# Optimization experiments

Measured on AMD Instinct MI355X. Metric: run time of the kernel, lower is better.

## Reference

```python
import jax, jax.numpy as jnp
import numpy as np

H = 32          # num_attention_heads
KVH = 8         # num_key_value_heads
D = 2048        # hidden_size
HD = D // H     # attention_head_size = 64
REP = H // KVH  # queries per kv head = 4


def setup_inputs() -> dict:
    key = jax.random.key(0)
    ks = jax.random.split(key, 7)
    s = 0.02
    return {
        "hidden_states": jax.random.normal(ks[0], (2, 2048, D), dtype=jnp.float32),
        "Wq": jax.random.normal(ks[1], (D, D), dtype=jnp.float32) * s,
        "bq": jax.random.normal(ks[2], (D,), dtype=jnp.float32) * s,
        "Wk": jax.random.normal(ks[3], (D, KVH * HD), dtype=jnp.float32) * s,
        "bk": jax.random.normal(ks[4], (KVH * HD,), dtype=jnp.float32) * s,
        "Wv": jax.random.normal(ks[5], (D, KVH * HD), dtype=jnp.float32) * s,
        "bv": jax.random.normal(ks[6], (KVH * HD,), dtype=jnp.float32) * s,
    }


def _split_heads(x, n_heads):
    # [B, S, n_heads*HD] -> [B, n_heads, S, HD]
    b, s, _ = x.shape
    return x.reshape(b, s, n_heads, HD).transpose(0, 2, 1, 3)


def reference(hidden_states, Wq, bq, Wk, bk, Wv, bv):
    b, s, _ = hidden_states.shape
    q = _split_heads(hidden_states @ Wq + bq, H)          # [B,H,S,HD]
    k = _split_heads(hidden_states @ Wk + bk, KVH)        # [B,KVH,S,HD]
    v = _split_heads(hidden_states @ Wv + bv, KVH)
    # repeat KV heads to match query heads (q_idx // REP -> kv_idx)
    k = jnp.repeat(k, REP, axis=1)                         # [B,H,S,HD]
    v = jnp.repeat(v, REP, axis=1)
    scores = jnp.einsum("bhqd,bhkd->bhqk", q, k) / jnp.sqrt(jnp.float32(HD))
    probs = jax.nn.softmax(scores, axis=-1)
    ctx = jnp.einsum("bhqk,bhkd->bhqd", probs, v)          # [B,H,S,HD]
    ctx = ctx.transpose(0, 2, 1, 3).reshape(b, s, H * HD)
    return ctx
```

## Files before the change

### kernel.cpp

```cpp
#include <hip/hip_runtime.h>
#include <hip/hip_bf16.h>

#define NH 32
#define NKVH 8
#define DMODEL 2048
#define HDIM 64
#define NB 2
#define SEQ 2048
#define MROWS (NB*SEQ)
#define NQ 2048
#define NKV 512
#define NTOT 3072
#define NT (SEQ/64)

typedef __bf16 bf16x4 __attribute__((ext_vector_type(4)));
typedef __bf16 bf16x8 __attribute__((ext_vector_type(8)));
typedef float  f32x2  __attribute__((ext_vector_type(2)));
typedef float  f32x4  __attribute__((ext_vector_type(4)));
typedef float  f32x16 __attribute__((ext_vector_type(16)));
typedef unsigned u32x2 __attribute__((ext_vector_type(2)));
typedef unsigned u32x4 __attribute__((ext_vector_type(4)));

__device__ inline __bf16 f2bf(float f) {
    unsigned u = __builtin_bit_cast(unsigned, f);
    u += 0x7fff + ((u >> 16) & 1);
    unsigned short s = (unsigned short)(u >> 16);
    return __builtin_bit_cast(__bf16, s);
}

__device__ inline unsigned pack2bf(float a, float b) {
    unsigned ua = __builtin_bit_cast(unsigned, a);
    ua += 0x7fff + ((ua >> 16) & 1);
    unsigned ub = __builtin_bit_cast(unsigned, b);
    ub += 0x7fff + ((ub >> 16) & 1);
    return (ua >> 16) | (ub & 0xffff0000u);
}

__device__ inline void gload_lds16(const void* g, void* l) {
    __builtin_amdgcn_global_load_lds(
        (const __attribute__((address_space(1))) void*)g,
        (__attribute__((address_space(3))) void*)l, 16, 0, 0);
}

__device__ inline float max3f(float a, float b, float c) {
    float r;
    asm("v_max3_f32 %0, %1, %2, %3" : "=v"(r) : "v"(a), "v"(b), "v"(c));
    return r;
}

__device__ inline float cross_max32(float x) {
#if __has_builtin(__builtin_amdgcn_permlane32_swap)
    unsigned xu = __builtin_bit_cast(unsigned, x);
    u32x2 r = __builtin_amdgcn_permlane32_swap(xu, xu, false, false);
    return fmaxf(__builtin_bit_cast(float, r[0]), __builtin_bit_cast(float, r[1]));
#else
    return fmaxf(x, __shfl_xor(x, 32));
#endif
}

__global__ __launch_bounds__(256)
void cvt_hs(const float* __restrict__ Hs, __bf16* __restrict__ Ab)
{
    size_t idx = ((size_t)blockIdx.x * 256 + threadIdx.x) * 8;
    f32x4 a = *reinterpret_cast<const f32x4*>(Hs + idx);
    f32x4 b = *reinterpret_cast<const f32x4*>(Hs + idx + 4);
    u32x4 w;
    w[0] = pack2bf(a[0], a[1]); w[1] = pack2bf(a[2], a[3]);
    w[2] = pack2bf(b[0], b[1]); w[3] = pack2bf(b[2], b[3]);
    *reinterpret_cast<u32x4*>((char*)Ab + idx * 2) = w;
}

__global__ __launch_bounds__(256)
void transpose_w(const float* __restrict__ Wq,
                 const float* __restrict__ Wk,
                 const float* __restrict__ Wv,
                 __bf16* __restrict__ Wt)
{
    __shared__ __bf16 tile[64][72];
    int k0 = blockIdx.x * 64;
    int n0 = blockIdx.y * 64;
    const float* Wsrc; int ncols; int nbase;
    if (n0 < NQ)            { Wsrc = Wq; ncols = NQ;  nbase = n0; }
    else if (n0 < NQ + NKV) { Wsrc = Wk; ncols = NKV; nbase = n0 - NQ; }
    else                    { Wsrc = Wv; ncols = NKV; nbase = n0 - NQ - NKV; }
    int t = threadIdx.x;
    int kl = t >> 2;
    int nc = (t & 3) * 16;
    const float* src = Wsrc + (size_t)(k0 + kl) * ncols + nbase + nc;
    #pragma unroll
    for (int i = 0; i < 4; ++i) {
        f32x4 v = *reinterpret_cast<const f32x4*>(src + i * 4);
        #pragma unroll
        for (int e = 0; e < 4; ++e) tile[kl][nc + i * 4 + e] = f2bf(v[e]);
    }
    __syncthreads();
    int nl = t >> 2;
    int kc = (t & 3) * 16;
    bf16x8 o0, o1;
    #pragma unroll
    for (int i = 0; i < 8; ++i) o0[i] = tile[kc + i][nl];
    #pragma unroll
    for (int i = 0; i < 8; ++i) o1[i] = tile[kc + 8 + i][nl];
    __bf16* dst = Wt + (size_t)(n0 + nl) * DMODEL + k0 + kc;
    *reinterpret_cast<bf16x8*>(dst)     = o0;
    *reinterpret_cast<bf16x8*>(dst + 8) = o1;
}

#define BM 128
#define BN 128
#define BK 64

__global__ __launch_bounds__(256)
void qkv_gemm(const __bf16* __restrict__ Ab,
              const __bf16* __restrict__ Wt,
              const float* __restrict__ bq,
              const float* __restrict__ bk,
              const float* __restrict__ bv,
              __bf16* __restrict__ Qb,
              __bf16* __restrict__ Kb,
              __bf16* __restrict__ Vt)
{
    __shared__ char lds[32768];

    int bid = blockIdx.x;
    int wg = (bid & 7) * 96 + (bid >> 3);
    int n0 = (wg % 24) * BN;
    int m0 = (wg / 24) * BM;

    int t = threadIdx.x;
    int wave = t >> 6, lane = t & 63;
    int g = lane >> 4, lh = lane & 15;
    int wr = wave >> 1, wc = wave & 1;

    int srow = wave * 8 + (lane >> 3);
    int schunk = (lane & 7) ^ (lane >> 3);
    const char* Asrc = (const char*)Ab + (size_t)(m0 + srow) * 4096 + schunk * 16;
    const char* Bsrc = (const char*)Wt + (size_t)(n0 + srow) * 4096 + schunk * 16;
    int dstw = wave * 1024;

    f32x4 acc[4][4] = {};

    for (int k0 = 0; k0 < DMODEL * 2; k0 += BK * 2) {
        #pragma unroll
        for (int i = 0; i < 4; ++i)
            gload_lds16(Asrc + (size_t)i * 32 * 4096 + k0, lds + i * 4096 + dstw);
        #pragma unroll
        for (int i = 0; i < 4; ++i)
            gload_lds16(Bsrc + (size_t)i * 32 * 4096 + k0, lds + 16384 + i * 4096 + dstw);
        __syncthreads();
        #pragma unroll
        for (int kk = 0; kk < 2; ++kk) {
            bf16x8 af[4], bfr[4];
            #pragma unroll
            for (int mi = 0; mi < 4; ++mi) {
                int row = wr * 64 + mi * 16 + lh;
                int byte = row * 128 + (((kk * 4 + g) ^ (lh & 7)) << 4);
                af[mi] = *reinterpret_cast<const bf16x8*>(lds + byte);
            }
            #pragma unroll
            for (int ni = 0; ni < 4; ++ni) {
                int row = wc * 64 + ni * 16 + lh;
                int byte = row * 128 + (((kk * 4 + g) ^ (lh & 7)) << 4);
                bfr[ni] = *reinterpret_cast<const bf16x8*>(lds + 16384 + byte);
            }
            #pragma unroll
            for (int mi = 0; mi < 4; ++mi)
                #pragma unroll
                for (int ni = 0; ni < 4; ++ni)
                    acc[mi][ni] = __builtin_amdgcn_mfma_f32_16x16x32_bf16(af[mi], bfr[ni], acc[mi][ni], 0, 0, 0);
        }
        __syncthreads();
    }

    int mode = (n0 < NQ) ? 0 : (n0 < NQ + NKV ? 1 : 2);
    const float* bias = (mode == 0) ? bq : (mode == 1 ? bk : bv);
    int nsub = (mode == 0) ? 0 : (mode == 1 ? NQ : NQ + NKV);
    float scale = (mode == 0) ? 0.18033688011112042f : 1.0f;

    float biasv[4];
    #pragma unroll
    for (int ni = 0; ni < 4; ++ni)
        biasv[ni] = bias[n0 - nsub + wc * 64 + ni * 16 + lh];

    int gsw = ((g & 1) << 1) | (g >> 1);

    #pragma unroll
    for (int mi = 0; mi < 4; ++mi) {
        #pragma unroll
        for (int j = 0; j < 4; ++j) {
            int m = m0 + wr * 64 + mi * 16 + 4 * g + j;
            int bb = m >> 11, s = m & (SEQ - 1);
            #pragma unroll
            for (int ni = 0; ni < 4; ++ni) {
                int n = n0 + wc * 64 + ni * 16 + lh;
                __bf16 val = f2bf((acc[mi][ni][j] + biasv[ni]) * scale);
                if (mode == 0) {
                    int hh = n >> 6, d = n & 63;
                    Qb[(((size_t)bb * NH + hh) * SEQ + s) * HDIM + d] = val;
                } else if (mode == 1) {
                    int nk = n - NQ; int kv = nk >> 6, d = nk & 63;
                    Kb[(((size_t)bb * NKVH + kv) * SEQ + s) * HDIM + d] = val;
                } else {
                    int nv = n - NQ - NKV; int kv = nv >> 6, d = nv & 63;
                    int sv = (s & ~12) | (gsw << 2);
                    Vt[(((size_t)bb * NKVH + kv) * HDIM + d) * SEQ + sv] = val;
                }
            }
        }
    }
}

#define SUBSTEP(BUFB, SS) do { \
    bf16x8 kf0_ = *reinterpret_cast<const bf16x8*>(lds + (BUFB) + koff[(SS)*4 + 0]); \
    bf16x8 kf1_ = *reinterpret_cast<const bf16x8*>(lds + (BUFB) + koff[(SS)*4 + 1]); \
    bf16x8 kf2_ = *reinterpret_cast<const bf16x8*>(lds + (BUFB) + koff[(SS)*4 + 2]); \
    bf16x8 kf3_ = *reinterpret_cast<const bf16x8*>(lds + (BUFB) + koff[(SS)*4 + 3]); \
    f32x16 s_ = {}; \
    __builtin_amdgcn_s_setprio(1); \
    s_ = __builtin_amdgcn_mfma_f32_32x32x16_bf16(kf0_, qf[0], s_, 0, 0, 0); \
    s_ = __builtin_amdgcn_mfma_f32_32x32x16_bf16(kf1_, qf[1], s_, 0, 0, 0); \
    s_ = __builtin_amdgcn_mfma_f32_32x32x16_bf16(kf2_, qf[2], s_, 0, 0, 0); \
    s_ = __builtin_amdgcn_mfma_f32_32x32x16_bf16(kf3_, qf[3], s_, 0, 0, 0); \
    __builtin_amdgcn_s_setprio(0); \
    float n0_ = max3f(max3f(s_[0], s_[1], s_[2]),  max3f(s_[3], s_[4], s_[5]), \
                      max3f(s_[6], s_[7], s_[8])); \
    float n1_ = max3f(max3f(s_[9], s_[10], s_[11]), max3f(s_[12], s_[13], s_[14]), s_[15]); \
    float mt_ = cross_max32(fmaxf(n0_, n1_)); \
    if (!__all(mt_ <= m_run + 8.0f)) { \
        float mn_ = fmaxf(m_run, mt_); \
        float al_ = __builtin_amdgcn_exp2f(m_run - mn_); \
        m_run = mn_; msub = -mn_; \
        accO0 *= al_; accO1 *= al_; lsum *= al_; \
    } \
    _Pragma("unroll") \
    for (int r = 0; r < 16; ++r) s_[r] = __builtin_amdgcn_exp2f(s_[r] + msub); \
    bf16x8 pa_, pb_; \
    _Pragma("unroll") \
    for (int e = 0; e < 8; ++e) { pa_[e] = (__bf16)s_[e]; pb_[e] = (__bf16)s_[8 + e]; } \
    bf16x8 va0_ = *reinterpret_cast<const bf16x8*>(lds + (BUFB) + 8192 + koff[2 * (SS)]); \
    bf16x8 vb0_ = *reinterpret_cast<const bf16x8*>(lds + (BUFB) + 8192 + koff[2 * (SS) + 1]); \
    bf16x8 va1_ = *reinterpret_cast<const bf16x8*>(lds + (BUFB) + 8192 + koff[4 + 2 * (SS)]); \
    bf16x8 vb1_ = *reinterpret_cast<const bf16x8*>(lds + (BUFB) + 8192 + koff[4 + 2 * (SS) + 1]); \
    __builtin_amdgcn_s_setprio(1); \
    accO0 = __builtin_amdgcn_mfma_f32_32x32x16_bf16(va0_, pa_, accO0, 0, 0, 0); \
    lsum  = __builtin_amdgcn_mfma_f32_32x32x16_bf16(ones, pa_, lsum,  0, 0, 0); \
    accO0 = __builtin_amdgcn_mfma_f32_32x32x16_bf16(vb0_, pb_, accO0, 0, 0, 0); \
    lsum  = __builtin_amdgcn_mfma_f32_32x32x16_bf16(ones, pb_, lsum,  0, 0, 0); \
    accO1 = __builtin_amdgcn_mfma_f32_32x32x16_bf16(va1_, pa_, accO1, 0, 0, 0); \
    accO1 = __builtin_amdgcn_mfma_f32_32x32x16_bf16(vb1_, pb_, accO1, 0, 0, 0); \
    __builtin_amdgcn_s_setprio(0); \
} while (0)

#define TILE(BUFB, NBUFB, KT, MORE) do { \
    if (MORE) { \
        gload_lds16(Kp + (size_t)((KT) + 1) * 8192 + kgoff, lds + (NBUFB) + kdst); \
        gload_lds16(Vp + (size_t)((KT) + 1) * 128 + vgoff,  lds + (NBUFB) + vdst); \
    } \
    SUBSTEP(BUFB, 0); \
    SUBSTEP(BUFB, 1); \
    __syncthreads(); \
} while (0)

__global__ __launch_bounds__(512, 4)
void attn(const __bf16* __restrict__ Qb,
          const __bf16* __restrict__ Kb,
          const __bf16* __restrict__ Vt,
          float* __restrict__ out)
{
    __shared__ char lds[32768];

    int qt = blockIdx.x;
    int bh = blockIdx.y;
    int b = bh >> 5, h = bh & 31;
    int kvh = h >> 2;
    int tid = threadIdx.x, wave = tid >> 6, lane = tid & 63;
    int ql = lane & 31, hi = lane >> 5;
    int q0 = qt * 256 + wave * 32;

    const __bf16* Qp = Qb + (size_t)(b * NH + h) * SEQ * HDIM;
    const char*   Kp = (const char*)(Kb + (size_t)(b * NKVH + kvh) * SEQ * HDIM);
    const char*   Vp = (const char*)(Vt + (size_t)(b * NKVH + kvh) * HDIM * SEQ);

    bf16x8 qf[4];
    #pragma unroll
    for (int f = 0; f < 4; ++f)
        qf[f] = *reinterpret_cast<const bf16x8*>(Qp + (size_t)(q0 + ql) * HDIM + f * 16 + hi * 8);

    u32x4 ou = { 0x3F803F80u, 0x3F803F80u, 0x3F803F80u, 0x3F803F80u };
    bf16x8 ones = __builtin_bit_cast(bf16x8, ou);

    int srow = tid >> 3;
    int schk = (tid & 7) ^ (srow & 7);
    int kgoff = srow * 128 + (schk << 4);
    size_t vgoff = (size_t)srow * (SEQ * 2) + (schk << 4);
    int kdst = tid * 16;
    int vdst = 8192 + tid * 16;

    int koff[8];
    #pragma unroll
    for (int kb = 0; kb < 2; ++kb)
        #pragma unroll
        for (int f = 0; f < 4; ++f)
            koff[kb * 4 + f] = (kb * 32 + ql) * 128 + ((f * 32 + hi * 16) ^ ((ql & 7) << 4));

    f32x16 accO0 = {}, accO1 = {}, lsum = {};
    float m_run = -1e30f, msub = 0.0f;

    gload_lds16(Kp + kgoff, lds + kdst);
    gload_lds16(Vp + vgoff, lds + vdst);
    __syncthreads();

    #pragma unroll 1
    for (int kt2 = 0; kt2 < 15; ++kt2) {
        TILE(0,     16384, 2 * kt2,     true);
        TILE(16384, 0,     2 * kt2 + 1, true);
    }
    TILE(0,     16384, 30, true);
    TILE(16384, 0,     31, false);

    float inv = 1.0f / lsum[0];
    float* op = out + ((size_t)b * SEQ + q0 + ql) * DMODEL + h * HDIM;
    #pragma unroll
    for (int G = 0; G < 4; ++G) {
        f32x4 o0 = { accO0[4 * G + 0] * inv, accO0[4 * G + 1] * inv,
                     accO0[4 * G + 2] * inv, accO0[4 * G + 3] * inv };
        f32x4 o1 = { accO1[4 * G + 0] * inv, accO1[4 * G + 1] * inv,
                     accO1[4 * G + 2] * inv, accO1[4 * G + 3] * inv };
        *reinterpret_cast<f32x4*>(op + 8 * G + 4 * hi)      = o0;
        *reinterpret_cast<f32x4*>(op + 32 + 8 * G + 4 * hi) = o1;
    }
}

extern "C" void kernel_launch(void* const* d_in, const int* in_sizes, int n_in,
                              void* d_out, int out_size, void* d_ws, size_t ws_size,
                              hipStream_t stream)
{
    const float* hs = (const float*)d_in[0];
    const float* Wq = (const float*)d_in[1];
    const float* bq = (const float*)d_in[2];
    const float* Wk = (const float*)d_in[3];
    const float* bk = (const float*)d_in[4];
    const float* Wv = (const float*)d_in[5];
    const float* bv = (const float*)d_in[6];
    float* out = (float*)d_out;

    char* ws = (char*)d_ws;
    __bf16* Wt = (__bf16*)(ws);
    __bf16* Ab = (__bf16*)(ws + 12582912);
    __bf16* Qb = (__bf16*)(ws + 12582912 + 16777216);
    __bf16* Kb = (__bf16*)(ws + 12582912 + 2*16777216);
    __bf16* Vt = (__bf16*)(ws + 12582912 + 2*16777216 + 4194304);

    hipLaunchKernelGGL(cvt_hs,      dim3(4096),   dim3(256), 0, stream, hs, Ab);
    hipLaunchKernelGGL(transpose_w, dim3(32, 48), dim3(256), 0, stream, Wq, Wk, Wv, Wt);
    hipLaunchKernelGGL(qkv_gemm,    dim3(768),    dim3(256), 0, stream, Ab, Wt, bq, bk, bv, Qb, Kb, Vt);
    hipLaunchKernelGGL(attn,        dim3(8, 64),  dim3(512), 0, stream, Qb, Kb, Vt, out);
}
```

Measured before the change: 179.7 us.

## Deepen attention K/V prefetch to four LDS buffers and remap GEMM tiles per XCD

The attention kernel moves from double buffering to a four-slot LDS ring (64 KB) and prefetches K/V two tiles ahead. The full __syncthreads is replaced by an explicit vmcnt wait plus a barrier, so one tile's loads can stay in flight across the barrier. Separately, the QKV GEMM block-to-tile mapping now gives each XCD a contiguous 8x12 region of M and N tiles to improve L2 reuse. The larger LDS footprint may reduce how many attention blocks fit per CU, which could offset the deeper prefetch.

```diff
diff --git a/kernel.cpp b/kernel.cpp
--- a/kernel.cpp
+++ b/kernel.cpp
@@ -123,9 +123,10 @@
     __shared__ char lds[32768];
 
     int bid = blockIdx.x;
-    int wg = (bid & 7) * 96 + (bid >> 3);
-    int n0 = (wg % 24) * BN;
-    int m0 = (wg / 24) * BM;
+    int xcd = bid & 7, r = bid >> 3;
+    int rm = r / 12, rn = r % 12;
+    int m0 = ((xcd >> 1) * 8 + rm) * BM;
+    int n0 = ((xcd & 1) * 12 + rn) * BN;
 
     int t = threadIdx.x;
     int wave = t >> 6, lane = t & 63;
@@ -251,14 +252,15 @@
     __builtin_amdgcn_s_setprio(0); \
 } while (0)
 
-#define TILE(BUFB, NBUFB, KT, MORE) do { \
-    if (MORE) { \
-        gload_lds16(Kp + (size_t)((KT) + 1) * 8192 + kgoff, lds + (NBUFB) + kdst); \
-        gload_lds16(Vp + (size_t)((KT) + 1) * 128 + vgoff,  lds + (NBUFB) + vdst); \
+#define TILE(BUFB, SBUFB, KT, STAGE, VM) do { \
+    if (STAGE) { \
+        gload_lds16(Kp + (size_t)((KT) + 2) * 8192 + kgoff, lds + (SBUFB) + kdst); \
+        gload_lds16(Vp + (size_t)((KT) + 2) * 128  + vgoff, lds + (SBUFB) + vdst); \
     } \
     SUBSTEP(BUFB, 0); \
     SUBSTEP(BUFB, 1); \
-    __syncthreads(); \
+    asm volatile("s_waitcnt vmcnt(" #VM ")" ::: "memory"); \
+    __builtin_amdgcn_s_barrier(); \
 } while (0)
 
 __global__ __launch_bounds__(512, 4)
@@ -267,7 +269,7 @@
           const __bf16* __restrict__ Vt,
           float* __restrict__ out)
 {
-    __shared__ char lds[32768];
+    __shared__ char lds[65536];
 
     int qt = blockIdx.x;
     int bh = blockIdx.y;
@@ -306,17 +308,25 @@
     f32x16 accO0 = {}, accO1 = {}, lsum = {};
     float m_run = -1e30f, msub = 0.0f;
 
-    gload_lds16(Kp + kgoff, lds + kdst);
-    gload_lds16(Vp + vgoff, lds + vdst);
-    __syncthreads();
+    gload_lds16(Kp + kgoff,        lds + kdst);
+    gload_lds16(Vp + vgoff,        lds + vdst);
+    gload_lds16(Kp + 8192 + kgoff, lds + 16384 + kdst);
+    gload_lds16(Vp + 128  + vgoff, lds + 16384 + vdst);
+    asm volatile("s_waitcnt vmcnt(2)" ::: "memory");
+    __builtin_amdgcn_s_barrier();
 
     #pragma unroll 1
-    for (int kt2 = 0; kt2 < 15; ++kt2) {
-        TILE(0,     16384, 2 * kt2,     true);
-        TILE(16384, 0,     2 * kt2 + 1, true);
-    }
-    TILE(0,     16384, 30, true);
-    TILE(16384, 0,     31, false);
+    for (int g4 = 0; g4 < 7; ++g4) {
+        int kt = g4 * 4;
+        TILE(0,     32768, kt + 0, true, 2);
+        TILE(16384, 49152, kt + 1, true, 2);
+        TILE(32768, 0,     kt + 2, true, 2);
+        TILE(49152, 16384, kt + 3, true, 2);
+    }
+    TILE(0,     32768, 28, true,  2);
+    TILE(16384, 49152, 29, true,  2);
+    TILE(32768, 0,     30, false, 0);
+    TILE(49152, 0,     31, false, 0);
 
     float inv = 1.0f / lsum[0];
     float* op = out + ((size_t)b * SEQ + q0 + ql) * DMODEL + h * HDIM;
```

After: 178.0 us. About the same (-1.0%).
